# Kernel tuning notes

Hardware: AMD Instinct MI355X
Metric: run time of the kernel (lower is better)

Reference implementation:

```python
import jax, jax.numpy as jnp
import numpy as np

B, S, HID = 2, 2048, 4096
H, KV, D = 32, 8, 128          # heads, kv heads, head_dim
G = H // KV                    # num_key_value_groups
THETA = 10000.0
SCALE = 1.0 / np.sqrt(D)
NEG_INF = -1e9


def rotate_half(x):
    x1, x2 = x[..., : D // 2], x[..., D // 2 :]
    return jnp.concatenate([-x2, x1], axis=-1)


def rope_tables(seq_len):
    inv_freq = 1.0 / (THETA ** (jnp.arange(0, D, 2, dtype=jnp.float32) / D))
    t = jnp.arange(seq_len, dtype=jnp.float32)
    freqs = jnp.outer(t, inv_freq)              # [S, D/2]
    emb = jnp.concatenate([freqs, freqs], -1)   # [S, D]
    return jnp.cos(emb), jnp.sin(emb)


def setup_inputs() -> dict:
    key = jax.random.key(0)
    ks = jax.random.split(key, 5)
    w = 0.02
    x = jax.random.normal(ks[0], (B, S, HID), jnp.float32)
    Wq = jax.random.normal(ks[1], (HID, H * D), jnp.float32) * w
    Wk = jax.random.normal(ks[2], (HID, KV * D), jnp.float32) * w
    Wv = jax.random.normal(ks[3], (HID, KV * D), jnp.float32) * w
    Wo = jax.random.normal(ks[4], (H * D, HID), jnp.float32) * w
    position_ids = jnp.broadcast_to(jnp.arange(S, dtype=jnp.int32), (B, S))
    causal = jnp.where(
        jnp.arange(S)[:, None] >= jnp.arange(S)[None, :], 0.0, NEG_INF
    ).astype(jnp.float32)
    attention_mask = jnp.broadcast_to(causal, (B, 1, S, S))
    return {
        "by_pass_hidden_states": x,
        "attention_mask": attention_mask,
        "position_ids": position_ids,
        "Wq": Wq,
        "Wk": Wk,
        "Wv": Wv,
        "Wo": Wo,
    }


def reference(by_pass_hidden_states, attention_mask, position_ids, Wq, Wk, Wv, Wo):
    x = by_pass_hidden_states
    # QKV projections (weights stored [in, out])
    q = (x @ Wq).reshape(B, S, H, D).transpose(0, 2, 1, 3)    # [B,H,S,D]
    k = (x @ Wk).reshape(B, S, KV, D).transpose(0, 2, 1, 3)   # [B,KV,S,D]
    v = (x @ Wv).reshape(B, S, KV, D).transpose(0, 2, 1, 3)   # [B,KV,S,D]
    # RoPE
    cos_t, sin_t = rope_tables(S)
    cos = cos_t[position_ids][:, None]   # [B,1,S,D]
    sin = sin_t[position_ids][:, None]
    q = q * cos + rotate_half(q) * sin
    k = k * cos + rotate_half(k) * sin
    # GQA attention without materializing repeated K/V: group query heads
    qg = q.reshape(B, KV, G, S, D)
    scores = jnp.einsum("bkgsd,bktd->bkgst", qg, k) * SCALE   # [B,KV,G,S,S]
    scores = scores.reshape(B, H, S, S) + attention_mask
    probs = jax.nn.softmax(scores.astype(jnp.float32), axis=-1).astype(x.dtype)
    ctx = jnp.einsum("bkgst,bktd->bkgsd", probs.reshape(B, KV, G, S, S), v)
    ctx = ctx.reshape(B, H, S, D).transpose(0, 2, 1, 3).reshape(B, S, H * D)
    return ctx @ Wo
```

## Files before the change

kernel.cpp:

```cpp
#include <hip/hip_runtime.h>
#include <cstdint>
#include <cstddef>

#define B_   2
#define S_   2048
#define HID_ 4096
#define H_   32
#define KV_  8
#define D_   128
#define M_   (B_*S_)
#define QSTR 6144

typedef __attribute__((ext_vector_type(8))) short bf16x8;
typedef __attribute__((ext_vector_type(4))) float f32x4;
typedef __attribute__((ext_vector_type(16))) float f32x16;
typedef __attribute__((ext_vector_type(4))) unsigned int u32x4;
typedef unsigned short u16;
typedef unsigned int   u32;

#define KSC (0.08838834764831845f * 1.4426950408889634f)

__device__ __forceinline__ float bf2f(u16 v){ u32 u = ((u32)v) << 16; return __builtin_bit_cast(float, u); }
__device__ __forceinline__ u16 f2bf(float f){
  u32 u = __builtin_bit_cast(u32, f);
  u32 r = u + 0x7fffu + ((u >> 16) & 1u);
  return (u16)(r >> 16);
}

__device__ __forceinline__ void gload_lds16(const void* g, void* lds){
  __builtin_amdgcn_global_load_lds(
      (const __attribute__((address_space(1))) void*)g,
      (__attribute__((address_space(3))) void*)lds, 16, 0, 0);
}

__global__ void cast_f32_bf16(const float* __restrict__ in, u16* __restrict__ out, int n){
  int i = (blockIdx.x * blockDim.x + threadIdx.x) * 4;
  if (i >= n) return;
  float4 v = *(const float4*)(in + i);
  ushort4 o;
  o.x = f2bf(v.x); o.y = f2bf(v.y); o.z = f2bf(v.z); o.w = f2bf(v.w);
  *(ushort4*)(out + i) = o;
}

__global__ __launch_bounds__(256) void tcast(const float* __restrict__ W, u16* __restrict__ WT,
                                             int Kd, int Nd){
  __shared__ __align__(16) u16 t[64][65];
  int k0 = blockIdx.x * 64, n0 = blockIdx.y * 64;
  int lx = threadIdx.x & 15, ly = threadIdx.x >> 4;
  #pragma unroll
  for (int rr = 0; rr < 4; ++rr){
    int r = rr * 16 + ly;
    float4 v = *(const float4*)(W + (size_t)(k0 + r) * Nd + n0 + lx * 4);
    t[lx*4+0][r] = f2bf(v.x);
    t[lx*4+1][r] = f2bf(v.y);
    t[lx*4+2][r] = f2bf(v.z);
    t[lx*4+3][r] = f2bf(v.w);
  }
  __syncthreads();
  #pragma unroll
  for (int rr = 0; rr < 4; ++rr){
    int r = rr * 16 + ly;
    ushort4 o;
    o.x = t[r][lx*4+0]; o.y = t[r][lx*4+1]; o.z = t[r][lx*4+2]; o.w = t[r][lx*4+3];
    *(ushort4*)(WT + (size_t)(n0 + r) * Kd + k0 + lx * 4) = o;
  }
}

__global__ __launch_bounds__(256) void vtrans(const u16* __restrict__ QKV, u16* __restrict__ Vt){
  __shared__ __align__(16) u16 t[64][65];
  int stile = blockIdx.x;
  int b = blockIdx.y >> 4, vt = blockIdx.y & 15;
  int s0 = stile * 64, c0 = vt * 64;
  int lx = threadIdx.x & 15, ly = threadIdx.x >> 4;
  #pragma unroll
  for (int rr = 0; rr < 4; ++rr){
    int r = rr * 16 + ly;
    ushort4 v = *(const ushort4*)(QKV + (size_t)(b*S_ + s0 + r) * QSTR + 5120 + c0 + lx*4);
    t[lx*4+0][r]=v.x; t[lx*4+1][r]=v.y; t[lx*4+2][r]=v.z; t[lx*4+3][r]=v.w;
  }
  __syncthreads();
  #pragma unroll
  for (int rr = 0; rr < 4; ++rr){
    int r = rr * 16 + ly;
    ushort4 o;
    o.x=t[r][lx*4+0]; o.y=t[r][lx*4+1]; o.z=t[r][lx*4+2]; o.w=t[r][lx*4+3];
    *(ushort4*)(Vt + (size_t)(b*1024 + c0 + r) * S_ + s0 + lx*4) = o;
  }
}

__global__ void rope_k(u16* __restrict__ X, const int* __restrict__ pos, int hshift, int stride){
  int idx = blockIdx.x * 256 + threadIdx.x;
  int i = idx & 63;
  int h = (idx >> 6) & ((1 << hshift) - 1);
  int t = idx >> (6 + hshift);
  u16* p0 = X + (size_t)t * stride + h * D_ + i;
  float x1 = bf2f(p0[0]), x2 = bf2f(p0[64]);
  float fpos = (float)pos[t];
  float invf = exp2f(-(float)(2 * i) * (13.287712379549449f / 128.0f));
  float f = fpos * invf;
  float sv = __sinf(f), cv = __cosf(f);
  p0[0]  = f2bf(x1 * cv - x2 * sv);
  p0[64] = f2bf(x2 * cv + x1 * sv);
}


#define SBAR() __builtin_amdgcn_sched_barrier(0)
#define BARX() do{ SBAR(); __builtin_amdgcn_s_barrier(); SBAR(); }while(0)

#define STG_A(PB, HALF, KT) do{ \
  gload_lds16(Ag + off0 + (size_t)(HALF)*1048576 + (size_t)(KT)*128, \
              (char*)smem + (PB)*32768 + (HALF)*16384 + w*1024); \
  gload_lds16(Ag + off0 + 524288 + (size_t)(HALF)*1048576 + (size_t)(KT)*128, \
              (char*)smem + (PB)*32768 + (HALF)*16384 + 8192 + w*1024); }while(0)
#define STG_B(PB, HALF, KT) do{ \
  gload_lds16(Bg + off0 + (size_t)(HALF)*1048576 + (size_t)(KT)*128, \
              (char*)smem + 65536 + (PB)*32768 + (HALF)*16384 + w*1024); \
  gload_lds16(Bg + off0 + 524288 + (size_t)(HALF)*1048576 + (size_t)(KT)*128, \
              (char*)smem + 65536 + (PB)*32768 + (HALF)*16384 + 8192 + w*1024); }while(0)

#define PHASE(P, MH, NH, ...) do{                                        \
  bf16x8 afr[2][4], bfr2[2][2];                                          \
  _Pragma("unroll") for (int ks = 0; ks < 2; ++ks){                      \
    _Pragma("unroll") for (int m = 0; m < 4; ++m)                        \
      afr[ks][m] = *(const bf16x8*)&smem[(P)*16384 + (MH)*8192 + aRowBase + m*1024 + csw[ks]]; \
    _Pragma("unroll") for (int n = 0; n < 2; ++n)                        \
      bfr2[ks][n] = *(const bf16x8*)&smem[32768 + (P)*16384 + (NH)*8192 + bRowBase + n*1024 + csw[ks]]; \
  }                                                                      \
  __VA_ARGS__;                                                           \
  BARX();                                                                \
  __builtin_amdgcn_s_setprio(1);                                         \
  _Pragma("unroll") for (int ks = 0; ks < 2; ++ks)                       \
    _Pragma("unroll") for (int m = 0; m < 4; ++m)                        \
      _Pragma("unroll") for (int n = 0; n < 2; ++n)                      \
        acc[(MH)*4+m][(NH)*2+n] = __builtin_amdgcn_mfma_f32_16x16x32_bf16(afr[ks][m], bfr2[ks][n], acc[(MH)*4+m][(NH)*2+n], 0, 0, 0); \
  __builtin_amdgcn_s_setprio(0);                                         \
}while(0)

template<bool OUTF32>
__global__ __launch_bounds__(512, 2) void gemm256(const u16* __restrict__ A, const u16* __restrict__ Bt,
                                                  void* __restrict__ C, int Nn, int mt){
  __shared__ __align__(16) u16 smem[65536];
  const int tid = threadIdx.x;
  const int l = tid & 63, w = tid >> 6;
  const int lr = l & 15, lk = l >> 4;
  const int wr = w >> 2, wc = w & 3;

  const int nwg = gridDim.x;
  const int sbid = ((int)blockIdx.x & 7) * (nwg >> 3) + ((int)blockIdx.x >> 3);
  const int bx = sbid % mt, by = sbid / mt;
  const size_t arow0 = (size_t)bx * 256;
  const size_t brow0 = (size_t)by * 256;
  const char* Ag = (const char*)(A + arow0 * 4096);
  const char* Bg = (const char*)(Bt + brow0 * 4096);

  const size_t off0 = (size_t)(w * 8 + (l >> 3)) * 8192 + (size_t)(((l & 7) ^ (l >> 3)) << 4);

  const int aRowBase = (wr*64 + lr) * 64;
  const int bRowBase = (wc*32 + lr) * 64;
  int csw[2];
  csw[0] = ((lk     ) ^ (lr & 7)) << 3;
  csw[1] = ((lk + 4) ^ (lr & 7)) << 3;

  f32x4 acc[8][4];
  #pragma unroll
  for (int i = 0; i < 8; ++i)
    #pragma unroll
    for (int j = 0; j < 4; ++j){ acc[i][j][0]=0.f; acc[i][j][1]=0.f; acc[i][j][2]=0.f; acc[i][j][3]=0.f; }

  STG_A(0, 0, 0); STG_B(0, 0, 0);
  STG_A(0, 1, 0); STG_B(0, 1, 0);
  STG_B(1, 0, 1); STG_A(1, 0, 1);
  asm volatile("s_waitcnt vmcnt(4)" ::: "memory");
  BARX();

  for (int t = 0; t < 64; ++t){
    const int P = t & 1;
    PHASE(P, 0, 0, { if (t < 63){ STG_A(P^1, 1, t+1); STG_B(P^1, 1, t+1); } });
    BARX();
    PHASE(P, 1, 0, {});
    BARX();
    PHASE(P, 0, 1, { if (t < 62){ STG_B(P, 0, t+2); } });
    BARX();
    PHASE(P, 1, 1, { if (t < 62){ STG_A(P, 0, t+2); } });
    if (t < 62) asm volatile("s_waitcnt vmcnt(4)" ::: "memory");
    else        asm volatile("s_waitcnt vmcnt(0)" ::: "memory");
    BARX();
  }

  #pragma unroll
  for (int mh = 0; mh < 2; ++mh)
    #pragma unroll
    for (int m = 0; m < 4; ++m)
      #pragma unroll
      for (int nh = 0; nh < 2; ++nh)
        #pragma unroll
        for (int n = 0; n < 2; ++n)
          #pragma unroll
          for (int j = 0; j < 4; ++j){
            size_t gr = arow0 + mh*128 + wr*64 + m*16 + lk*4 + j;
            size_t gc = brow0 + nh*128 + wc*32 + n*16 + lr;
            float v = acc[mh*4+m][nh*2+n][j];
            if (OUTF32) ((float*)C)[gr * Nn + gc] = v;
            else        ((u16*)C)[gr * Nn + gc] = f2bf(v);
          }
}

__global__ __launch_bounds__(512, 2) void attn_k(const u16* __restrict__ QKV,
                                                 const u16* __restrict__ Vtg,
                                                 u16* __restrict__ ctx){
  __shared__ __align__(16) u16 smem[32768];
  const int tid = threadIdx.x;
  const int l = tid & 63, w = tid >> 6;
  const int lane31 = l & 31, hi = l >> 5;
  const int hb = blockIdx.x;
  const int b = hb >> 5, h = hb & 31, kvh = h >> 2;
  const int qb = 7 - blockIdx.y;
  const int q0w = qb * 256 + w * 32;
  const int qg = q0w + lane31;

  const u16* Qp = QKV + (size_t)b * S_ * QSTR + (size_t)h * D_;
  const char* Kp = (const char*)(QKV + (size_t)b * S_ * QSTR + 4096 + (size_t)kvh * D_);
  const char* Vp = (const char*)(Vtg + ((size_t)b * 1024 + kvh * 128) * S_);

  bf16x8 qf[8];
  #pragma unroll
  for (int dt = 0; dt < 8; ++dt)
    qf[dt] = *(const bf16x8*)(Qp + (size_t)qg * QSTR + dt * 16 + hi * 8);

  const int krow0 = (2*w)*4 + (l >> 4), krow1 = krow0 + 4;
  const size_t koff0 = (size_t)krow0 * (QSTR*2) + (((l & 15) << 4) ^ ((krow0 & 7) << 4));
  const size_t koff1 = (size_t)krow1 * (QSTR*2) + (((l & 15) << 4) ^ ((krow1 & 7) << 4));
  const int vrow0 = (2*w)*8 + (l >> 3), vrow1 = vrow0 + 8;
  const size_t voff0 = (size_t)vrow0 * (S_*2) + (((l & 7) << 4) ^ ((vrow0 & 7) << 4));
  const size_t voff1 = (size_t)vrow1 * (S_*2) + (((l & 7) << 4) ^ ((vrow1 & 7) << 4));

  f32x16 acc[4];
  #pragma unroll
  for (int dt = 0; dt < 4; ++dt)
    #pragma unroll
    for (int i = 0; i < 16; ++i) acc[dt][i] = 0.f;
  float mrow = -3e38f, lsum = 0.f;

  const int nt = qb * 4 + 4;

  auto STAGE = [&](int t, int bufn){
    char* Kb = (char*)smem + bufn * 16384;
    char* Vb = (char*)smem + 32768 + bufn * 16384;
    size_t kb = (size_t)t * 64 * (QSTR*2);
    size_t vb = (size_t)t * 128;
    gload_lds16(Kp + kb + koff0, Kb + (2*w)*1024);
    gload_lds16(Kp + kb + koff1, Kb + (2*w+1)*1024);
    gload_lds16(Vp + vb + voff0, Vb + (2*w)*1024);
    gload_lds16(Vp + vb + voff1, Vb + (2*w+1)*1024);
  };

  STAGE(0, 0);
  __syncthreads();
  int buf = 0;
  for (int t = 0; t < nt; ++t){
    if (t + 1 < nt) STAGE(t + 1, buf ^ 1);
    const int kbase = t * 64;
    if (kbase <= q0w + 31){
      const char* Kb = (const char*)smem + buf * 16384;
      const char* Vb = (const char*)smem + 32768 + buf * 16384;
      const int swz = (lane31 & 7) << 4;

      f32x16 s0, s1;
      #pragma unroll
      for (int i = 0; i < 16; ++i){ s0[i] = 0.f; s1[i] = 0.f; }
      #pragma unroll
      for (int dt = 0; dt < 8; ++dt){
        bf16x8 kf = *(const bf16x8*)(Kb + lane31*256 + ((dt*32 + hi*16) ^ swz));
        s0 = __builtin_amdgcn_mfma_f32_32x32x16_bf16(kf, qf[dt], s0, 0, 0, 0);
      }
      #pragma unroll
      for (int dt = 0; dt < 8; ++dt){
        bf16x8 kf = *(const bf16x8*)(Kb + (32 + lane31)*256 + ((dt*32 + hi*16) ^ swz));
        s1 = __builtin_amdgcn_mfma_f32_32x32x16_bf16(kf, qf[dt], s1, 0, 0, 0);
      }

      if (kbase + 63 > q0w){
        int thr = qg - kbase;
        #pragma unroll
        for (int r = 0; r < 16; ++r){
          int kc = (r & 3) + 8*(r >> 2) + 4*hi;
          s0[r] = (kc > thr)      ? -1e30f : s0[r];
          s1[r] = (kc + 32 > thr) ? -1e30f : s1[r];
        }
      }

      float tmax = s0[0];
      #pragma unroll
      for (int r = 1; r < 16; ++r) tmax = fmaxf(tmax, s0[r]);
      #pragma unroll
      for (int r = 0; r < 16; ++r) tmax = fmaxf(tmax, s1[r]);
      tmax = fmaxf(tmax, __shfl_xor(tmax, 32));
      float mn = fmaxf(mrow, tmax);
      float rf = exp2f((mrow - mn) * KSC);
      mrow = mn;
      float ps = 0.f;
      #pragma unroll
      for (int r = 0; r < 16; ++r){
        float a = exp2f((s0[r] - mn) * KSC);
        float c = exp2f((s1[r] - mn) * KSC);
        s0[r] = a; s1[r] = c; ps += a + c;
      }
      ps += __shfl_xor(ps, 32);
      lsum = lsum * rf + ps;
      #pragma unroll
      for (int dt = 0; dt < 4; ++dt)
        #pragma unroll
        for (int i = 0; i < 16; ++i) acc[dt][i] *= rf;

      u32 pw[16];
      #pragma unroll
      for (int g = 0; g < 4; ++g){
        pw[2*g]     = (u32)f2bf(s0[4*g])   | ((u32)f2bf(s0[4*g+1]) << 16);
        pw[2*g+1]   = (u32)f2bf(s0[4*g+2]) | ((u32)f2bf(s0[4*g+3]) << 16);
        pw[8+2*g]   = (u32)f2bf(s1[4*g])   | ((u32)f2bf(s1[4*g+1]) << 16);
        pw[8+2*g+1] = (u32)f2bf(s1[4*g+2]) | ((u32)f2bf(s1[4*g+3]) << 16);
      }

      #pragma unroll
      for (int kt = 0; kt < 4; ++kt){
        u32 W0 = pw[kt*4+0], W1 = pw[kt*4+1], W2 = pw[kt*4+2], W3 = pw[kt*4+3];
        u32 x0 = hi ? W0 : W2;
        u32 x1 = hi ? W1 : W3;
        u32 y0 = __shfl_xor(x0, 32);
        u32 y1 = __shfl_xor(x1, 32);
        u32 w0 = hi ? y0 : W0;
        u32 w1 = hi ? y1 : W1;
        u32 w2 = hi ? W2 : y0;
        u32 w3 = hi ? W3 : y1;
        u32x4 pk; pk[0]=w0; pk[1]=w1; pk[2]=w2; pk[3]=w3;
        bf16x8 pa = __builtin_bit_cast(bf16x8, pk);
        #pragma unroll
        for (int dt = 0; dt < 4; ++dt){
          bf16x8 vf = *(const bf16x8*)(Vb + (dt*32 + lane31)*128 + ((kt*32 + hi*16) ^ swz));
          acc[dt] = __builtin_amdgcn_mfma_f32_32x32x16_bf16(vf, pa, acc[dt], 0, 0, 0);
        }
      }
    }
    __syncthreads();
    buf ^= 1;
  }

  __syncthreads();
  u16* Ot = smem + w * 4096;
  float inv = 1.f / lsum;
  #pragma unroll
  for (int dt = 0; dt < 4; ++dt)
    #pragma unroll
    for (int r = 0; r < 16; ++r){
      int d = dt*32 + (r & 3) + 8*(r >> 2) + 4*hi;
      Ot[lane31*128 + (d ^ ((lane31 & 15) << 2))] = f2bf(acc[dt][r] * inv);
    }
  u16* outp = ctx + ((size_t)(b * S_ + q0w)) * HID_ + h * D_;
  #pragma unroll
  for (int it = 0; it < 16; ++it){
    int id = it * 64 + l;
    int q = id >> 5;
    int c4 = (id & 31) * 4;
    ushort4 vv = *(const ushort4*)(Ot + q*128 + (c4 ^ ((q & 15) << 2)));
    *(ushort4*)(outp + (size_t)q * HID_ + c4) = vv;
  }
}

extern "C" void kernel_launch(void* const* d_in, const int* in_sizes, int n_in,
                              void* d_out, int out_size, void* d_ws, size_t ws_size,
                              hipStream_t stream) {
  const float* x  = (const float*)d_in[0];
  const int*   pos = (const int*)d_in[2];
  const float* Wq = (const float*)d_in[3];
  const float* Wk = (const float*)d_in[4];
  const float* Wv = (const float*)d_in[5];
  const float* Wo = (const float*)d_in[6];

  char* ws = (char*)d_ws;
  u16* xb   = (u16*)(ws);
  u16* WT   = (u16*)(ws + ((size_t)32 << 20));
  u16* WoT  = (u16*)(ws + ((size_t)80 << 20));
  u16* QKVb = (u16*)(ws + ((size_t)112 << 20));
  u16* Vtg  = (u16*)(ws + ((size_t)32 << 20));

  cast_f32_bf16<<<16384, 256, 0, stream>>>(x, xb, HID_ * M_);
  tcast<<<dim3(64, 64), 256, 0, stream>>>(Wq, WT, 4096, 4096);
  tcast<<<dim3(64, 16), 256, 0, stream>>>(Wk, WT + (size_t)4096 * 4096, 4096, 1024);
  tcast<<<dim3(64, 16), 256, 0, stream>>>(Wv, WT + (size_t)5120 * 4096, 4096, 1024);
  tcast<<<dim3(64, 64), 256, 0, stream>>>(Wo, WoT, 4096, 4096);
  gemm256<false><<<16 * 24, 512, 0, stream>>>(xb, WT, QKVb, 6144, 16);
  rope_k<<<32768, 256, 0, stream>>>(QKVb,        pos, 5, QSTR);
  rope_k<<<8192,  256, 0, stream>>>(QKVb + 4096, pos, 3, QSTR);
  vtrans<<<dim3(32, 32), 256, 0, stream>>>(QKVb, Vtg);
  attn_k<<<dim3(64, 8), 512, 0, stream>>>(QKVb, Vtg, xb);
  gemm256<true><<<16 * 16, 512, 0, stream>>>(xb, WoT, d_out, 4096, 16);
}
```

Measured before the change: 588.3 us.

## Keep A/B fragments in registers across GEMM phases and deepen LDS prefetch

Restructures the 256x256 GEMM main loop so A and B LDS fragments are read once per k-step and reused across the four MFMA quadrants in a zig-zag order (A0B0, A1B0, A1B1, A0B1), instead of reloading both operands per phase. Prefetch now stages the whole k+2 tile into the same ping-pong buffer half by half as each half is consumed, and waits with a deeper outstanding-load count. This is meant to cut LDS read traffic and overlap global loads with compute further, at the cost of more live VGPRs and extra barriers.

```diff
diff --git a/kernel.cpp b/kernel.cpp
--- a/kernel.cpp
+++ b/kernel.cpp
@@ -118,23 +118,28 @@
   gload_lds16(Bg + off0 + 524288 + (size_t)(HALF)*1048576 + (size_t)(KT)*128, \
               (char*)smem + 65536 + (PB)*32768 + (HALF)*16384 + 8192 + w*1024); }while(0)
 
-#define PHASE(P, MH, NH, ...) do{                                        \
-  bf16x8 afr[2][4], bfr2[2][2];                                          \
-  _Pragma("unroll") for (int ks = 0; ks < 2; ++ks){                      \
-    _Pragma("unroll") for (int m = 0; m < 4; ++m)                        \
-      afr[ks][m] = *(const bf16x8*)&smem[(P)*16384 + (MH)*8192 + aRowBase + m*1024 + csw[ks]]; \
-    _Pragma("unroll") for (int n = 0; n < 2; ++n)                        \
-      bfr2[ks][n] = *(const bf16x8*)&smem[32768 + (P)*16384 + (NH)*8192 + bRowBase + n*1024 + csw[ks]]; \
-  }                                                                      \
-  __VA_ARGS__;                                                           \
-  BARX();                                                                \
-  __builtin_amdgcn_s_setprio(1);                                         \
-  _Pragma("unroll") for (int ks = 0; ks < 2; ++ks)                       \
-    _Pragma("unroll") for (int m = 0; m < 4; ++m)                        \
-      _Pragma("unroll") for (int n = 0; n < 2; ++n)                      \
-        acc[(MH)*4+m][(NH)*2+n] = __builtin_amdgcn_mfma_f32_16x16x32_bf16(afr[ks][m], bfr2[ks][n], acc[(MH)*4+m][(NH)*2+n], 0, 0, 0); \
-  __builtin_amdgcn_s_setprio(0);                                         \
-}while(0)
+#define RD_A(DST, HALF) do{ \
+  _Pragma("unroll") for (int ks = 0; ks < 2; ++ks) \
+  _Pragma("unroll") for (int m = 0; m < 4; ++m) \
+    DST[ks][m] = *(const bf16x8*)&smem[P*16384 + (HALF)*8192 + aRowBase + m*1024 + csw[ks]]; }while(0)
+#define RD_B(DST, HALF) do{ \
+  _Pragma("unroll") for (int ks = 0; ks < 2; ++ks) \
+  _Pragma("unroll") for (int n = 0; n < 2; ++n) \
+    DST[ks][n] = *(const bf16x8*)&smem[32768 + P*16384 + (HALF)*8192 + bRowBase + n*1024 + csw[ks]]; }while(0)
+
+template<int MO, int NO>
+__device__ __forceinline__ void mfma_quad(f32x4 (&acc)[8][4],
+                                          const bf16x8 (&af)[2][4], const bf16x8 (&bf)[2][2]){
+  __builtin_amdgcn_s_setprio(1);
+  #pragma unroll
+  for (int ks = 0; ks < 2; ++ks)
+    #pragma unroll
+    for (int m = 0; m < 4; ++m)
+      #pragma unroll
+      for (int n = 0; n < 2; ++n)
+        acc[MO+m][NO+n] = __builtin_amdgcn_mfma_f32_16x16x32_bf16(af[ks][m], bf[ks][n], acc[MO+m][NO+n], 0, 0, 0);
+  __builtin_amdgcn_s_setprio(0);
+}
 
 template<bool OUTF32>
 __global__ __launch_bounds__(512, 2) void gemm256(const u16* __restrict__ A, const u16* __restrict__ Bt,
@@ -167,23 +172,33 @@
     #pragma unroll
     for (int j = 0; j < 4; ++j){ acc[i][j][0]=0.f; acc[i][j][1]=0.f; acc[i][j][2]=0.f; acc[i][j][3]=0.f; }
 
-  STG_A(0, 0, 0); STG_B(0, 0, 0);
-  STG_A(0, 1, 0); STG_B(0, 1, 0);
-  STG_B(1, 0, 1); STG_A(1, 0, 1);
-  asm volatile("s_waitcnt vmcnt(4)" ::: "memory");
+  STG_A(0, 0, 0); STG_B(0, 0, 0); STG_A(0, 1, 0); STG_B(0, 1, 0);
+  STG_A(1, 0, 1); STG_B(1, 0, 1); STG_A(1, 1, 1); STG_B(1, 1, 1);
+  asm volatile("s_waitcnt vmcnt(8)" ::: "memory");
   BARX();
 
   for (int t = 0; t < 64; ++t){
     const int P = t & 1;
-    PHASE(P, 0, 0, { if (t < 63){ STG_A(P^1, 1, t+1); STG_B(P^1, 1, t+1); } });
-    BARX();
-    PHASE(P, 1, 0, {});
-    BARX();
-    PHASE(P, 0, 1, { if (t < 62){ STG_B(P, 0, t+2); } });
-    BARX();
-    PHASE(P, 1, 1, { if (t < 62){ STG_A(P, 0, t+2); } });
-    if (t < 62) asm volatile("s_waitcnt vmcnt(4)" ::: "memory");
-    else        asm volatile("s_waitcnt vmcnt(0)" ::: "memory");
+    bf16x8 a0h[2][4], a1[2][4], b0[2][2], b1[2][2];
+    RD_A(a0h, 0); RD_B(b0, 0);
+    BARX();
+    mfma_quad<0,0>(acc, a0h, b0);
+    BARX();
+    if (t < 62){ STG_A(P, 0, t+2); STG_B(P, 0, t+2); }
+    RD_A(a1, 1);
+    BARX();
+    mfma_quad<4,0>(acc, a1, b0);
+    BARX();
+    if (t < 62){ STG_A(P, 1, t+2); }
+    RD_B(b1, 1);
+    BARX();
+    mfma_quad<4,2>(acc, a1, b1);
+    BARX();
+    if (t < 62){ STG_B(P, 1, t+2); }
+    BARX();
+    mfma_quad<0,2>(acc, a0h, b1);
+    if (t < 62)      asm volatile("s_waitcnt vmcnt(8)" ::: "memory");
+    else if (t < 63) asm volatile("s_waitcnt vmcnt(0)" ::: "memory");
     BARX();
   }
 
```

After: 546.9 us. 1.08x faster.
